# Kernel optimization log

Measured on AMD Instinct MI355X. Metric: run time of the kernel, lower is better.

The kernel has to match this reference:

```python
import jax, jax.numpy as jnp
from jax import lax
import numpy as np

T, B, IN, H = 192, 16, 256, 256


def setup_inputs() -> dict:
    key = jax.random.key(0)
    ks = jax.random.split(key, 8)
    s = 0.05  # small init scale to keep gates well-conditioned
    return {
        "x": jax.random.normal(ks[0], (T, B, IN), dtype=jnp.float32),
        # shared LSTM (PyTorch gate order i,f,g,o)
        "W_ih": jax.random.normal(ks[1], (4 * H, IN), dtype=jnp.float32) * s,
        "W_hh": jax.random.normal(ks[2], (4 * H, H), dtype=jnp.float32) * s,
        "b_lstm": jnp.zeros((4 * H,), dtype=jnp.float32),
        # additive attention: Ws: (IN+2H)->H, Us: H->1
        "Ws_w": jax.random.normal(ks[3], (H, IN + 2 * H), dtype=jnp.float32) * s,
        "Ws_b": jnp.zeros((H,), dtype=jnp.float32),
        "Us_w": jax.random.normal(ks[4], (1, H), dtype=jnp.float32) * s,
        "Us_b": jnp.zeros((1,), dtype=jnp.float32),
        # task-specific message LSTM cell: gates from concat(x_t, Rt, h_prev)
        "Wc": jax.random.normal(ks[5], (4 * H, IN + 2 * H), dtype=jnp.float32) * s,
        "bc": jnp.zeros((4 * H,), dtype=jnp.float32),
        "TASK": 0,
    }


def _lstm_gates(pre, c):
    i, f, g, o = jnp.split(pre, 4, axis=-1)
    i = jax.nn.sigmoid(i)
    f = jax.nn.sigmoid(f)
    g = jnp.tanh(g)
    o = jax.nn.sigmoid(o)
    c_new = f * c + i * g
    h_new = o * jnp.tanh(c_new)
    return h_new, c_new


def reference(x, W_ih, W_hh, b_lstm, Ws_w, Ws_b, Us_w, Us_b, Wc, bc, TASK):
    t_len, b, _ = x.shape
    h = W_hh.shape[1]

    h0 = jnp.zeros((b, h), x.dtype)

    # ---- shared LSTM over time ----
    def shared_step(carry, xt):
        hh, cc = carry
        pre = xt @ W_ih.T + hh @ W_hh.T + b_lstm
        hh, cc = _lstm_gates(pre, cc)
        return (hh, cc), hh

    (_, _), hs = lax.scan(shared_step, (h0, h0), x)  # hs: [T,B,H]

    # ---- per-timestep additive attention + message LSTM cell ----
    def task_step(carry, xt):
        hh, cc = carry
        h_task = jnp.broadcast_to(hh[None], (t_len, b, h))
        cat = jnp.concatenate([hs, h_task, x], axis=-1)          # [T,B,IN+2H]
        score = jnp.tanh(cat @ Ws_w.T + Ws_b) @ Us_w.T + Us_b    # [T,B,1]
        att = jax.nn.softmax(score, axis=0)                       # over time
        Rt = jnp.sum(att * hs, axis=0)                            # [B,H]
        pre = jnp.concatenate([xt, Rt, hh], axis=-1) @ Wc.T + bc
        hh, cc = _lstm_gates(pre, cc)
        return (hh, cc), hh

    (_, _), outs = lax.scan(task_step, (h0, h0), x)  # [T,B,H]
    return jnp.transpose(outs, (1, 0, 2))  # [B,T,H] (torch.stack axis=1)
```

## Files before the change

### kernel.cpp

```cpp
#include <hip/hip_runtime.h>
#include <hip/hip_fp16.h>

#define T_LEN 192

typedef unsigned long long u64;
typedef _Float16 f16x8 __attribute__((ext_vector_type(8)));
typedef float f32x4 __attribute__((ext_vector_type(4)));

#define OFF_X1F   0
#define OFF_XPRE  3145728
#define OFF_XB3   6291456
#define OFF_HSB   7077888
#define OFF_P     7864320
#define OFF_H     7921664
#define OFF_HX    7929856
#define OFF_HP    7946240
#define EXCH_WORDS 147456

#define SMEM_TASK 148736

__device__ __forceinline__ unsigned packh2(float a, float b){
  union { __half2 h; unsigned u; } v;
  v.h = __halves2half2(__float2half(a), __float2half(b));
  return v.u;
}
__device__ __forceinline__ float2 unp2(unsigned u){
  union { unsigned u32; __half2 h; } v; v.u32 = u;
  return __half22float2(v.h);
}
__device__ __forceinline__ float fdot2(unsigned a, unsigned b, float c){
#if __has_builtin(__builtin_amdgcn_fdot2)
  typedef _Float16 h2t __attribute__((ext_vector_type(2)));
  union { unsigned u; h2t h; } ua, ub;
  ua.u = a; ub.u = b;
  return __builtin_amdgcn_fdot2(ua.h, ub.h, c, false);
#else
  float2 x = unp2(a), y = unp2(b);
  return c + x.x*y.x + x.y*y.y;
#endif
}
__device__ __forceinline__ float tanh_f(float x){
  float cx = fminf(fmaxf(x, -15.f), 15.f);
  float e = __expf(2.f * cx);
  return (e - 1.f) / (e + 1.f);
}
__device__ __forceinline__ float sigm(float x){
  float cx = fminf(fmaxf(x, -30.f), 30.f);
  return 1.f / (1.f + __expf(-cx));
}

__device__ __forceinline__ u64 gld64(const u64* p){
  return __hip_atomic_load(p, __ATOMIC_RELAXED, __HIP_MEMORY_SCOPE_AGENT);
}
__device__ __forceinline__ void gst64(u64* p, u64 v){
  __hip_atomic_store(p, v, __ATOMIC_RELAXED, __HIP_MEMORY_SCOPE_AGENT);
}

__global__ __launch_bounds__(256) void initk(float* p, int n){
  int i = blockIdx.x * blockDim.x + threadIdx.x;
  int stride = gridDim.x * blockDim.x;
  for (; i < n; i += stride) p[i] = 0.f;
}

__global__ __launch_bounds__(256) void proj3m(const float* __restrict__ x,
                                              const float* __restrict__ W_ih,
                                              const float* __restrict__ b_l,
                                              const float* __restrict__ Wc,
                                              const float* __restrict__ bc,
                                              const float* __restrict__ Ws_w,
                                              const float* __restrict__ Ws_b,
                                              float* __restrict__ ws){
  __shared__ unsigned xhi[16 * 136];
  __shared__ unsigned xlo[16 * 136];
  const int bx = blockIdx.x, t = blockIdx.y, tid = threadIdx.x;

  {
    int row = tid >> 4, c0 = (tid & 15) * 16;
    const float* xp = &x[(t * 16 + row) * 256 + c0];
    #pragma unroll
    for (int i = 0; i < 8; ++i) {
      float2 v = *(const float2*)&xp[2 * i];
      _Float16 h0 = (_Float16)v.x, h1 = (_Float16)v.y;
      float l0 = v.x - (float)h0, l1 = v.y - (float)h1;
      union { _Float16 h[2]; unsigned u; } ph, pl;
      ph.h[0] = h0; ph.h[1] = h1;
      pl.h[0] = (_Float16)l0; pl.h[1] = (_Float16)l1;
      xhi[row * 136 + c0 / 2 + i] = ph.u;
      xlo[row * 136 + c0 / 2 + i] = pl.u;
    }
  }

  const int wave = tid >> 6, lane = tid & 63;
  const int b16 = lane & 15, quad = lane >> 4;
  const int n0 = bx * 64 + wave * 16;
  const float* wrow; const float* bias; int nb, mode;
  if (bx < 16)      { nb = n0;        wrow = &W_ih[(nb + b16) * 256];       bias = b_l;  mode = 0; }
  else if (bx < 32) { nb = n0 - 1024; wrow = &Wc[(nb + b16) * 768];         bias = bc;   mode = 1; }
  else              { nb = n0 - 2048; wrow = &Ws_w[(nb + b16) * 768 + 512]; bias = Ws_b; mode = 2; }

  f16x8 whi[8], wlo[8];
  #pragma unroll
  for (int kk = 0; kk < 8; ++kk) {
    const float* wp = wrow + kk * 32 + quad * 8;
    f16x8 h, l;
    #pragma unroll
    for (int j = 0; j < 8; ++j) {
      float v = wp[j];
      _Float16 hh = (_Float16)v;
      h[j] = hh; l[j] = (_Float16)(v - (float)hh);
    }
    whi[kk] = h; wlo[kk] = l;
  }
  f32x4 acc;
  #pragma unroll
  for (int r = 0; r < 4; ++r) acc[r] = bias[nb + quad * 4 + r];
  __syncthreads();

  #pragma unroll
  for (int kk = 0; kk < 8; ++kk) {
    union { uint4 u; f16x8 h; } bh, bl;
    bh.u = *(const uint4*)&xhi[b16 * 136 + kk * 16 + quad * 4];
    bl.u = *(const uint4*)&xlo[b16 * 136 + kk * 16 + quad * 4];
    acc = __builtin_amdgcn_mfma_f32_16x16x32_f16(whi[kk], bh.h, acc, 0, 0, 0);
    acc = __builtin_amdgcn_mfma_f32_16x16x32_f16(wlo[kk], bh.h, acc, 0, 0, 0);
    acc = __builtin_amdgcn_mfma_f32_16x16x32_f16(whi[kk], bl.h, acc, 0, 0, 0);
  }

  float4 res; res.x = acc[0]; res.y = acc[1]; res.z = acc[2]; res.w = acc[3];
  if (mode == 0) {
    *(float4*)&ws[OFF_X1F + (((u64)t * 64 + (n0 >> 4)) * 16 + b16) * 16 + quad * 4] = res;
  } else if (mode == 1) {
    *(float4*)&ws[OFF_XPRE + ((u64)t * 16 + b16) * 1024 + nb + quad * 4] = res;
  } else {
    *(float4*)&ws[OFF_XB3 + ((u64)t * 16 + b16) * 256 + nb + quad * 4] = res;
  }
}

__global__ __launch_bounds__(512) void lstm_kernel(const float* __restrict__ X1F,
                                                   const float* __restrict__ W_hh,
                                                   float* __restrict__ hsB,
                                                   u64* __restrict__ hx){
  __shared__ unsigned hT[16 * 136];
  const int tid = threadIdx.x;
  const int wg = blockIdx.x;
  const int wave = tid >> 6, lane = tid & 63;
  const int b16 = lane & 15, quad = lane >> 4;
  const int jb = wg * 8 + wave;
  const int peerbase = (1 - wg) * 64;

  f16x8 wf[4][8];
  #pragma unroll
  for (int g = 0; g < 4; ++g) {
    #pragma unroll
    for (int kk = 0; kk < 8; ++kk) {
      int row = g * 256 + jb * 16 + b16;
      const float* wp = &W_hh[row * 256 + kk * 32 + quad * 8];
      f16x8 v;
      #pragma unroll
      for (int j = 0; j < 8; ++j) v[j] = (_Float16)wp[j];
      wf[g][kk] = v;
    }
  }
  for (int i = tid; i < 16 * 136; i += 512) hT[i] = 0u;
  float cst[4] = {0.f, 0.f, 0.f, 0.f};
  __syncthreads();

  for (int t = 0; t < T_LEN; ++t) {
    float4 xi[4];
    #pragma unroll
    for (int g = 0; g < 4; ++g)
      xi[g] = *(const float4*)&X1F[((t * 64 + g * 16 + jb) * 16 + b16) * 16 + quad * 4];

    if (t > 0) {
      const u64* src = &hx[((u64)((t - 1) & 1)) * 2048];
      int bbq = tid >> 5, k2 = tid & 31;
      int jp0 = peerbase + 2 * k2;
      u64 v0, v1;
      for (;;) {
        v0 = gld64(&src[bbq * 128 + jp0]);
        v1 = gld64(&src[bbq * 128 + jp0 + 1]);
        if ((unsigned)v0 == (unsigned)t && (unsigned)v1 == (unsigned)t) break;
      }
      hT[bbq * 136 + jp0]     = (unsigned)(v0 >> 32);
      hT[bbq * 136 + jp0 + 1] = (unsigned)(v1 >> 32);
    }
    __syncthreads();

    f32x4 acc[4];
    #pragma unroll
    for (int g = 0; g < 4; ++g) {
      f32x4 a; a[0]=xi[g].x; a[1]=xi[g].y; a[2]=xi[g].z; a[3]=xi[g].w;
      acc[g] = a;
    }
    #pragma unroll
    for (int kk = 0; kk < 8; ++kk) {
      union { uint4 u; f16x8 h; } bv;
      bv.u = *(const uint4*)&hT[b16 * 136 + kk * 16 + quad * 4];
      #pragma unroll
      for (int g = 0; g < 4; ++g)
        acc[g] = __builtin_amdgcn_mfma_f32_16x16x32_f16(wf[g][kk], bv.h, acc[g], 0, 0, 0);
    }
    __syncthreads();

    float hv[4];
    #pragma unroll
    for (int r = 0; r < 4; ++r) {
      float pi = acc[0][r], pf = acc[1][r], pg = acc[2][r], po = acc[3][r];
      float cn = fmaf(sigm(pf), cst[r], sigm(pi) * tanh_f(pg));
      hv[r] = sigm(po) * tanh_f(cn);
      cst[r] = cn;
    }
    int j0 = jb * 16 + quad * 4;
    int jp = j0 >> 1;
    unsigned p01 = packh2(hv[0], hv[1]);
    unsigned p23 = packh2(hv[2], hv[3]);
    u64* dst = &hx[((u64)(t & 1)) * 2048];
    gst64(&dst[b16 * 128 + jp],     ((u64)p01 << 32) | (unsigned)(t + 1));
    gst64(&dst[b16 * 128 + jp + 1], ((u64)p23 << 32) | (unsigned)(t + 1));
    *(float4*)&hsB[(b16 * 192 + t) * 256 + j0] = make_float4(hv[0], hv[1], hv[2], hv[3]);
    hT[b16 * 136 + jp]     = p01;
    hT[b16 * 136 + jp + 1] = p23;
  }
}

__global__ __launch_bounds__(1024) void task_kernel(
    const float* __restrict__ xb3, const float* __restrict__ xpre,
    const float* __restrict__ hsB, const float* __restrict__ Us_w,
    const float* __restrict__ Us_b, const float* __restrict__ Wc,
    const float* __restrict__ Ws_w,
    u64* __restrict__ Pbuf, u64* __restrict__ Hbuf, u64* __restrict__ HPbuf,
    float* __restrict__ out){
  extern __shared__ char smem[];
  unsigned* hsL  = (unsigned*)smem;
  unsigned* Ws1L = (unsigned*)(smem + 99072);
  float*    baseS= (float*)(smem + 115584);
  unsigned* WcH  = (unsigned*)smem;
  unsigned* Ws2P = (unsigned*)(smem + 65536);
  float* prel    = (float*)(smem + 82944);
  float* eel     = (float*)(smem + 89600);
  unsigned* h2l  = (unsigned*)(smem + 90368);
  unsigned* h2own= (unsigned*)(smem + 90880);
  float* hterml  = (float*)(smem + 90944);
  float* usl     = (float*)(smem + 91072);
  float* msc     = (float*)(smem + 91200);
  unsigned* G2   = (unsigned*)(smem + 99072);

  const int tid = threadIdx.x;
  const int bb = blockIdx.x & 15;
  const int s  = blockIdx.x >> 4;

  for (int idx = tid; idx < 24576; idx += 1024) {
    int tp = idx >> 7, k2 = idx & 127;
    const float* hp = &hsB[(bb * 192 + tp) * 256 + 2 * k2];
    hsL[tp * 129 + k2] = packh2(hp[0], hp[1]);
  }
  for (int idx = tid; idx < 4096; idx += 1024) {
    int c = idx >> 7, k2 = idx & 127;
    const float* wp = &Ws_w[(32 * s + c) * 768 + 2 * k2];
    Ws1L[c * 129 + k2] = packh2(wp[0], wp[1]);
  }
  __syncthreads();
  {
    int c = tid & 31, g = tid >> 5;
    float a6[6];
    #pragma unroll
    for (int j = 0; j < 6; ++j)
      a6[j] = xb3[((g * 6 + j) * 16 + bb) * 256 + 32 * s + c];
    for (int k2 = 0; k2 < 128; ++k2) {
      unsigned wv = Ws1L[c * 129 + k2];
      #pragma unroll
      for (int j = 0; j < 6; ++j)
        a6[j] = fdot2(wv, hsL[(g * 6 + j) * 129 + k2], a6[j]);
    }
    #pragma unroll
    for (int j = 0; j < 6; ++j)
      baseS[(g * 6 + j) * 33 + c] = a6[j];
  }
  __syncthreads();
  unsigned bs4[4] = {0u, 0u, 0u, 0u};
  if (tid < 768) {
    int tp = tid >> 2, q = tid & 3;
    #pragma unroll
    for (int j2 = 0; j2 < 4; ++j2)
      bs4[j2] = packh2(baseS[tp * 33 + q * 8 + 2 * j2],
                       baseS[tp * 33 + q * 8 + 2 * j2 + 1]);
  }
  __syncthreads();
  {
    int l = tid & 127, tg = tid >> 7;
    int row = (l >> 5) * 256 + 32 * s + (l & 31);
    const float* wr = &Wc[row * 768 + 256];
    float acc[24];
    #pragma unroll
    for (int i = 0; i < 24; ++i) acc[i] = 0.f;
    for (int kc = 0; kc < 128; kc += 16) {
      unsigned wv[16];
      #pragma unroll
      for (int i = 0; i < 16; ++i) {
        float2 wp2 = *(const float2*)&wr[2 * (kc + i)];
        wv[i] = packh2(wp2.x, wp2.y);
      }
      #pragma unroll
      for (int tt = 0; tt < 24; ++tt) {
        const unsigned* hp = &hsL[(tg * 24 + tt) * 129 + kc];
        float a = acc[tt];
        #pragma unroll
        for (int i = 0; i < 16; ++i) a = fdot2(wv[i], hp[i], a);
        acc[tt] = a;
      }
    }
    #pragma unroll
    for (int i = 0; i < 12; ++i)
      G2[l * 97 + tg * 12 + i] = packh2(acc[2 * i], acc[2 * i + 1]);
  }
  __syncthreads();
  for (int idx = tid; idx < 16384; idx += 1024) {
    int j = idx & 3, l = (idx >> 2) & 127, k2q = idx >> 9;
    int k2 = k2q * 4 + j;
    int row = (l >> 5) * 256 + 32 * s + (l & 31);
    const float* wp = &Wc[row * 768 + 512 + 2 * k2];
    WcH[idx] = packh2(wp[0], wp[1]);
  }
  for (int idx = tid; idx < 4096; idx += 1024) {
    int c = idx >> 4, j = idx & 15;
    const float* wp = &Ws_w[c * 768 + 256 + 2 * (16 * s + j)];
    Ws2P[c * 17 + j] = packh2(wp[0], wp[1]);
  }
  if (tid < 32) usl[tid] = Us_w[32 * s + tid];
  const float usb = Us_b[0];
  __syncthreads();

  u64* Pb  = Pbuf + (bb * 8) * 192;
  u64* Hb  = Hbuf + bb * 256;
  u64* HPb = HPbuf + (bb * 8) * 256;
  const uint4* wp4 = (const uint4*)WcH;
  const uint4* av4 = (const uint4*)h2l;
  float creg = 0.f;

  for (int t = 0; t < T_LEN; ++t) {
    const unsigned seq = (unsigned)(t + 1);
    float xp0 = 0.f, xp1 = 0.f, xp2 = 0.f, xp3 = 0.f;
    if (tid < 32) {
      const float* xq = &xpre[(t * 16 + bb) * 1024 + 32 * s + tid];
      xp0 = xq[0]; xp1 = xq[256]; xp2 = xq[512]; xp3 = xq[768];
    }
    if (t > 0) {
      if (tid < 256) {
        int c = tid >> 3, sp = tid & 7;
        u64 v;
        do { v = gld64(&HPb[sp * 256 + 32 * s + c]); } while ((unsigned)v != (unsigned)t);
        float a = __uint_as_float((unsigned)(v >> 32));
        a += __shfl_xor(a, 1); a += __shfl_xor(a, 2); a += __shfl_xor(a, 4);
        if (sp == 0) hterml[c] = a;
      } else if (tid < 512) {
        int col = tid - 256;
        u64 v;
        do { v = gld64(&Hb[col]); } while ((unsigned)v != (unsigned)t);
        float hvv = __uint_as_float((unsigned)(v >> 32));
        float hp_ = __shfl_xor(hvv, 1);
        if ((col & 1) == 0) h2l[col >> 1] = packh2(hvv, hp_);
      }
    } else {
      if (tid < 32) hterml[tid] = 0.f;
      if (tid < 128) h2l[tid] = 0u;
    }
    __syncthreads();
    if (tid < 768) {
      int tp = tid >> 2, q = tid & 3;
      float p = 0.f;
      #pragma unroll
      for (int m = 0; m < 4; ++m) {
        float2 bv = unp2(bs4[m]);
        int c0 = q * 8 + 2 * m;
        p += usl[c0]     * tanh_f(bv.x + hterml[c0]);
        p += usl[c0 + 1] * tanh_f(bv.y + hterml[c0 + 1]);
      }
      p += __shfl_xor(p, 1);
      p += __shfl_xor(p, 2);
      if ((tid & 3) == 0)
        gst64(&Pb[s * 192 + tp], ((u64)__float_as_uint(p) << 32) | seq);
    }
    {
      int l = tid & 127, kq = tid >> 7;
      float a = 0.f;
      #pragma unroll
      for (int i = 0; i < 4; ++i) {
        uint4 w4 = wp4[(kq * 4 + i) * 128 + l];
        uint4 a4 = av4[kq * 4 + i];
        a = fdot2(w4.x, a4.x, a); a = fdot2(w4.y, a4.y, a);
        a = fdot2(w4.z, a4.z, a); a = fdot2(w4.w, a4.w, a);
      }
      prel[l * 13 + kq] = a;
    }
    if (tid < 192) {
      u64 v[8];
      for (;;) {
        bool ok = true;
        #pragma unroll
        for (int sp = 0; sp < 8; ++sp) {
          v[sp] = gld64(&Pb[sp * 192 + tid]);
          ok &= ((unsigned)v[sp] == seq);
        }
        if (ok) break;
      }
      float sum = 0.f;
      #pragma unroll
      for (int sp = 0; sp < 8; ++sp) sum += __uint_as_float((unsigned)(v[sp] >> 32));
      eel[tid] = __expf(sum + usb);
    }
    __syncthreads();
    if (tid < 64) {
      float aa = eel[tid] + eel[tid + 64] + eel[tid + 128];
      #pragma unroll
      for (int off = 32; off >= 1; off >>= 1) aa += __shfl_xor(aa, off);
      if (tid == 0) msc[0] = 1.f / aa;
    }
    if (tid >= 512) {
      int l = (tid - 512) & 127, tq = (tid - 512) >> 7;
      const unsigned* gp = &G2[l * 97 + tq * 24];
      const float2* ep = (const float2*)&eel[tq * 48];
      float a = 0.f;
      #pragma unroll
      for (int i = 0; i < 24; ++i) {
        float2 g = unp2(gp[i]);
        float2 e = ep[i];
        a = fmaf(g.x, e.x, a); a = fmaf(g.y, e.y, a);
      }
      prel[l * 13 + 8 + tq] = a;
    }
    __syncthreads();
    if (tid < 32) {
      float m = msc[0];
      float pr[4];
      #pragma unroll
      for (int g = 0; g < 4; ++g) {
        const float* pp = &prel[(g * 32 + tid) * 13];
        float hsum = pp[0] + pp[1] + pp[2] + pp[3] + pp[4] + pp[5] + pp[6] + pp[7];
        float gsum = pp[8] + pp[9] + pp[10] + pp[11];
        pr[g] = hsum + m * gsum;
      }
      pr[0] += xp0; pr[1] += xp1; pr[2] += xp2; pr[3] += xp3;
      float cn = fmaf(sigm(pr[1]), creg, sigm(pr[0]) * tanh_f(pr[2]));
      float hh = sigm(pr[3]) * tanh_f(cn);
      creg = cn;
      gst64(&Hb[32 * s + tid], ((u64)__float_as_uint(hh) << 32) | seq);
      out[(bb * 192 + t) * 256 + 32 * s + tid] = hh;
      float hp_ = __shfl_xor(hh, 1);
      if ((tid & 1) == 0) h2own[tid >> 1] = packh2(hh, hp_);
    }
    __syncthreads();
    if (tid < 256) {
      float a = 0.f;
      const unsigned* wp = &Ws2P[tid * 17];
      #pragma unroll
      for (int j = 0; j < 16; ++j) a = fdot2(wp[j], h2own[j], a);
      gst64(&HPb[s * 256 + tid], ((u64)__float_as_uint(a) << 32) | seq);
    }
  }
}

extern "C" void kernel_launch(void* const* d_in, const int* in_sizes, int n_in,
                              void* d_out, int out_size, void* d_ws, size_t ws_size,
                              hipStream_t stream) {
  (void)in_sizes; (void)n_in; (void)out_size; (void)ws_size;
  const float* x    = (const float*)d_in[0];
  const float* W_ih = (const float*)d_in[1];
  const float* W_hh = (const float*)d_in[2];
  const float* b_l  = (const float*)d_in[3];
  const float* Ws_w = (const float*)d_in[4];
  const float* Ws_b = (const float*)d_in[5];
  const float* Us_w = (const float*)d_in[6];
  const float* Us_b = (const float*)d_in[7];
  const float* Wc   = (const float*)d_in[8];
  const float* bc   = (const float*)d_in[9];
  float* out = (float*)d_out;
  float* ws = (float*)d_ws;

  hipFuncSetAttribute((const void*)task_kernel,
                      hipFuncAttributeMaxDynamicSharedMemorySize, 160 * 1024);

  initk<<<64, 256, 0, stream>>>(ws + OFF_P, EXCH_WORDS);

  proj3m<<<dim3(36, 192), 256, 0, stream>>>(x, W_ih, b_l, Wc, bc, Ws_w, Ws_b, ws);

  lstm_kernel<<<2, 512, 0, stream>>>(ws + OFF_X1F, W_hh, ws + OFF_HSB,
                                     (u64*)(ws + OFF_HX));

  task_kernel<<<128, 1024, SMEM_TASK, stream>>>(
      ws + OFF_XB3, ws + OFF_XPRE, ws + OFF_HSB, Us_w, Us_b, Wc, Ws_w,
      (u64*)(ws + OFF_P), (u64*)(ws + OFF_H), (u64*)(ws + OFF_HP), out);
}
```

Measured before the change: 1.653 ms.

## Replace cross-block MFMA LSTM with per-batch independent blocks using fdot2

The shared LSTM recurrence previously ran on 2 workgroups that exchanged hidden state through global memory with spin-wait flags every timestep. It now runs one 1024-thread block per batch element, with no inter-block sync. Each thread computes one gate pre-activation via fp16 fdot2 against a pre-converted, transposed fp16 W_hh that is streamed from global or L2 each step. The projection kernel also processes two timesteps per block so its weight fragments are reused, and the X1F layout changes accordingly. This removes the cross-block polling latency, but every block now re-reads the 512KB fp16 weight matrix each step instead of keeping it in registers.

```diff
diff --git a/kernel.cpp b/kernel.cpp
--- a/kernel.cpp
+++ b/kernel.cpp
@@ -13,8 +13,8 @@
 #define OFF_HSB   7077888
 #define OFF_P     7864320
 #define OFF_H     7921664
-#define OFF_HX    7929856
 #define OFF_HP    7946240
+#define OFF_WHH   8011776
 #define EXCH_WORDS 147456
 
 #define SMEM_TASK 148736
@@ -62,6 +62,17 @@
   for (; i < n; i += stride) p[i] = 0.f;
 }
 
+__global__ __launch_bounds__(512) void whhc(const float* __restrict__ W_hh,
+                                            uint4* __restrict__ w4t){
+  int idx = blockIdx.x * 512 + threadIdx.x;
+  int j = idx >> 5, ko = idx & 31;
+  const float* wp = &W_hh[j * 256 + ko * 8];
+  uint4 v;
+  v.x = packh2(wp[0], wp[1]); v.y = packh2(wp[2], wp[3]);
+  v.z = packh2(wp[4], wp[5]); v.w = packh2(wp[6], wp[7]);
+  w4t[ko * 1024 + j] = v;
+}
+
 __global__ __launch_bounds__(256) void proj3m(const float* __restrict__ x,
                                               const float* __restrict__ W_ih,
                                               const float* __restrict__ b_l,
@@ -70,13 +81,14 @@
                                               const float* __restrict__ Ws_w,
                                               const float* __restrict__ Ws_b,
                                               float* __restrict__ ws){
-  __shared__ unsigned xhi[16 * 136];
-  __shared__ unsigned xlo[16 * 136];
-  const int bx = blockIdx.x, t = blockIdx.y, tid = threadIdx.x;
-
-  {
+  __shared__ unsigned xhi[2][16 * 136];
+  __shared__ unsigned xlo[2][16 * 136];
+  const int bx = blockIdx.x, t0 = blockIdx.y * 2, tid = threadIdx.x;
+
+  #pragma unroll
+  for (int tt = 0; tt < 2; ++tt) {
     int row = tid >> 4, c0 = (tid & 15) * 16;
-    const float* xp = &x[(t * 16 + row) * 256 + c0];
+    const float* xp = &x[((t0 + tt) * 16 + row) * 256 + c0];
     #pragma unroll
     for (int i = 0; i < 8; ++i) {
       float2 v = *(const float2*)&xp[2 * i];
@@ -85,8 +97,8 @@
       union { _Float16 h[2]; unsigned u; } ph, pl;
       ph.h[0] = h0; ph.h[1] = h1;
       pl.h[0] = (_Float16)l0; pl.h[1] = (_Float16)l1;
-      xhi[row * 136 + c0 / 2 + i] = ph.u;
-      xlo[row * 136 + c0 / 2 + i] = pl.u;
+      xhi[tt][row * 136 + c0 / 2 + i] = ph.u;
+      xlo[tt][row * 136 + c0 / 2 + i] = pl.u;
     }
   }
 
@@ -111,115 +123,73 @@
     }
     whi[kk] = h; wlo[kk] = l;
   }
-  f32x4 acc;
+  f32x4 acc[2];
   #pragma unroll
-  for (int r = 0; r < 4; ++r) acc[r] = bias[nb + quad * 4 + r];
+  for (int tt = 0; tt < 2; ++tt)
+    #pragma unroll
+    for (int r = 0; r < 4; ++r) acc[tt][r] = bias[nb + quad * 4 + r];
   __syncthreads();
 
   #pragma unroll
   for (int kk = 0; kk < 8; ++kk) {
-    union { uint4 u; f16x8 h; } bh, bl;
-    bh.u = *(const uint4*)&xhi[b16 * 136 + kk * 16 + quad * 4];
-    bl.u = *(const uint4*)&xlo[b16 * 136 + kk * 16 + quad * 4];
-    acc = __builtin_amdgcn_mfma_f32_16x16x32_f16(whi[kk], bh.h, acc, 0, 0, 0);
-    acc = __builtin_amdgcn_mfma_f32_16x16x32_f16(wlo[kk], bh.h, acc, 0, 0, 0);
-    acc = __builtin_amdgcn_mfma_f32_16x16x32_f16(whi[kk], bl.h, acc, 0, 0, 0);
-  }
-
-  float4 res; res.x = acc[0]; res.y = acc[1]; res.z = acc[2]; res.w = acc[3];
-  if (mode == 0) {
-    *(float4*)&ws[OFF_X1F + (((u64)t * 64 + (n0 >> 4)) * 16 + b16) * 16 + quad * 4] = res;
-  } else if (mode == 1) {
-    *(float4*)&ws[OFF_XPRE + ((u64)t * 16 + b16) * 1024 + nb + quad * 4] = res;
-  } else {
-    *(float4*)&ws[OFF_XB3 + ((u64)t * 16 + b16) * 256 + nb + quad * 4] = res;
-  }
-}
-
-__global__ __launch_bounds__(512) void lstm_kernel(const float* __restrict__ X1F,
-                                                   const float* __restrict__ W_hh,
-                                                   float* __restrict__ hsB,
-                                                   u64* __restrict__ hx){
-  __shared__ unsigned hT[16 * 136];
+    #pragma unroll
+    for (int tt = 0; tt < 2; ++tt) {
+      union { uint4 u; f16x8 h; } bh, bl;
+      bh.u = *(const uint4*)&xhi[tt][b16 * 136 + kk * 16 + quad * 4];
+      bl.u = *(const uint4*)&xlo[tt][b16 * 136 + kk * 16 + quad * 4];
+      acc[tt] = __builtin_amdgcn_mfma_f32_16x16x32_f16(whi[kk], bh.h, acc[tt], 0, 0, 0);
+      acc[tt] = __builtin_amdgcn_mfma_f32_16x16x32_f16(wlo[kk], bh.h, acc[tt], 0, 0, 0);
+      acc[tt] = __builtin_amdgcn_mfma_f32_16x16x32_f16(whi[kk], bl.h, acc[tt], 0, 0, 0);
+    }
+  }
+
+  #pragma unroll
+  for (int tt = 0; tt < 2; ++tt) {
+    int t = t0 + tt;
+    float4 res; res.x = acc[tt][0]; res.y = acc[tt][1]; res.z = acc[tt][2]; res.w = acc[tt][3];
+    if (mode == 0) {
+      *(float4*)&ws[OFF_X1F + ((u64)t * 16 + b16) * 1024 + nb + quad * 4] = res;
+    } else if (mode == 1) {
+      *(float4*)&ws[OFF_XPRE + ((u64)t * 16 + b16) * 1024 + nb + quad * 4] = res;
+    } else {
+      *(float4*)&ws[OFF_XB3 + ((u64)t * 16 + b16) * 256 + nb + quad * 4] = res;
+    }
+  }
+}
+
+__global__ __launch_bounds__(1024) void lstm_b(const float* __restrict__ x1,
+                                               const uint4* __restrict__ w4t,
+                                               float* __restrict__ hsB){
+  __shared__ uint4 h4l[32];
+  __shared__ float pre[1024];
   const int tid = threadIdx.x;
-  const int wg = blockIdx.x;
-  const int wave = tid >> 6, lane = tid & 63;
-  const int b16 = lane & 15, quad = lane >> 4;
-  const int jb = wg * 8 + wave;
-  const int peerbase = (1 - wg) * 64;
-
-  f16x8 wf[4][8];
-  #pragma unroll
-  for (int g = 0; g < 4; ++g) {
-    #pragma unroll
-    for (int kk = 0; kk < 8; ++kk) {
-      int row = g * 256 + jb * 16 + b16;
-      const float* wp = &W_hh[row * 256 + kk * 32 + quad * 8];
-      f16x8 v;
-      #pragma unroll
-      for (int j = 0; j < 8; ++j) v[j] = (_Float16)wp[j];
-      wf[g][kk] = v;
-    }
-  }
-  for (int i = tid; i < 16 * 136; i += 512) hT[i] = 0u;
-  float cst[4] = {0.f, 0.f, 0.f, 0.f};
-  __syncthreads();
+  const int bb = blockIdx.x;
+  float cst = 0.f;
+  if (tid < 32) h4l[tid] = make_uint4(0u, 0u, 0u, 0u);
+  __syncthreads();
+  const uint4* wrow = w4t + tid;
 
   for (int t = 0; t < T_LEN; ++t) {
-    float4 xi[4];
-    #pragma unroll
-    for (int g = 0; g < 4; ++g)
-      xi[g] = *(const float4*)&X1F[((t * 64 + g * 16 + jb) * 16 + b16) * 16 + quad * 4];
-
-    if (t > 0) {
-      const u64* src = &hx[((u64)((t - 1) & 1)) * 2048];
-      int bbq = tid >> 5, k2 = tid & 31;
-      int jp0 = peerbase + 2 * k2;
-      u64 v0, v1;
-      for (;;) {
-        v0 = gld64(&src[bbq * 128 + jp0]);
-        v1 = gld64(&src[bbq * 128 + jp0 + 1]);
-        if ((unsigned)v0 == (unsigned)t && (unsigned)v1 == (unsigned)t) break;
-      }
-      hT[bbq * 136 + jp0]     = (unsigned)(v0 >> 32);
-      hT[bbq * 136 + jp0 + 1] = (unsigned)(v1 >> 32);
-    }
-    __syncthreads();
-
-    f32x4 acc[4];
-    #pragma unroll
-    for (int g = 0; g < 4; ++g) {
-      f32x4 a; a[0]=xi[g].x; a[1]=xi[g].y; a[2]=xi[g].z; a[3]=xi[g].w;
-      acc[g] = a;
-    }
-    #pragma unroll
-    for (int kk = 0; kk < 8; ++kk) {
-      union { uint4 u; f16x8 h; } bv;
-      bv.u = *(const uint4*)&hT[b16 * 136 + kk * 16 + quad * 4];
-      #pragma unroll
-      for (int g = 0; g < 4; ++g)
-        acc[g] = __builtin_amdgcn_mfma_f32_16x16x32_f16(wf[g][kk], bv.h, acc[g], 0, 0, 0);
-    }
-    __syncthreads();
-
-    float hv[4];
-    #pragma unroll
-    for (int r = 0; r < 4; ++r) {
-      float pi = acc[0][r], pf = acc[1][r], pg = acc[2][r], po = acc[3][r];
-      float cn = fmaf(sigm(pf), cst[r], sigm(pi) * tanh_f(pg));
-      hv[r] = sigm(po) * tanh_f(cn);
-      cst[r] = cn;
-    }
-    int j0 = jb * 16 + quad * 4;
-    int jp = j0 >> 1;
-    unsigned p01 = packh2(hv[0], hv[1]);
-    unsigned p23 = packh2(hv[2], hv[3]);
-    u64* dst = &hx[((u64)(t & 1)) * 2048];
-    gst64(&dst[b16 * 128 + jp],     ((u64)p01 << 32) | (unsigned)(t + 1));
-    gst64(&dst[b16 * 128 + jp + 1], ((u64)p23 << 32) | (unsigned)(t + 1));
-    *(float4*)&hsB[(b16 * 192 + t) * 256 + j0] = make_float4(hv[0], hv[1], hv[2], hv[3]);
-    hT[b16 * 136 + jp]     = p01;
-    hT[b16 * 136 + jp + 1] = p23;
+    float a = x1[(t * 16 + bb) * 1024 + tid];
+    #pragma unroll 8
+    for (int ko = 0; ko < 32; ++ko) {
+      uint4 w = wrow[ko * 1024];
+      uint4 hv = h4l[ko];
+      a = fdot2(w.x, hv.x, a); a = fdot2(w.y, hv.y, a);
+      a = fdot2(w.z, hv.z, a); a = fdot2(w.w, hv.w, a);
+    }
+    pre[tid] = a;
+    __syncthreads();
+    if (tid < 256) {
+      float pi = pre[tid], pf = pre[tid + 256], pg = pre[tid + 512], po = pre[tid + 768];
+      float cn = fmaf(sigm(pf), cst, sigm(pi) * tanh_f(pg));
+      float hh = sigm(po) * tanh_f(cn);
+      cst = cn;
+      hsB[(bb * 192 + t) * 256 + tid] = hh;
+      float hp_ = __shfl_xor(hh, 1);
+      if ((tid & 1) == 0) ((unsigned*)h4l)[tid >> 1] = packh2(hh, hp_);
+    }
+    __syncthreads();
   }
 }
 
@@ -481,10 +451,12 @@
 
   initk<<<64, 256, 0, stream>>>(ws + OFF_P, EXCH_WORDS);
 
-  proj3m<<<dim3(36, 192), 256, 0, stream>>>(x, W_ih, b_l, Wc, bc, Ws_w, Ws_b, ws);
-
-  lstm_kernel<<<2, 512, 0, stream>>>(ws + OFF_X1F, W_hh, ws + OFF_HSB,
-                                     (u64*)(ws + OFF_HX));
+  whhc<<<64, 512, 0, stream>>>(W_hh, (uint4*)(ws + OFF_WHH));
+
+  proj3m<<<dim3(36, 96), 256, 0, stream>>>(x, W_ih, b_l, Wc, bc, Ws_w, Ws_b, ws);
+
+  lstm_b<<<16, 1024, 0, stream>>>(ws + OFF_X1F, (const uint4*)(ws + OFF_WHH),
+                                  ws + OFF_HSB);
 
   task_kernel<<<128, 1024, SMEM_TASK, stream>>>(
       ws + OFF_XB3, ws + OFF_XPRE, ws + OFF_HSB, Us_w, Us_b, Wc, Ws_w,
```

Result: slower. 1.866 ms (+12.9%).

## Overlap Wc/Ws projections with the recurrent LSTM and split its h-matmul

Applied to the files above, without the earlier changes.

The input projection kernel is split. The W_ih part stays as its own kernel, now processing two timesteps per block to reuse the converted weights. The Wc and Ws projections move into extra blocks of the LSTM launch, so they run on otherwise idle CUs while the two recurrent blocks step through time. Inside the recurrence, the MFMA half that uses the block's own hidden slice is issued before spinning on the peer's slice, which hides part of the exchange latency. This adds barrier and ordering changes, and it depends on the two LSTM blocks being scheduled alongside the 960 projection blocks, which must not starve them.

```diff
diff --git a/kernel.cpp b/kernel.cpp
--- a/kernel.cpp
+++ b/kernel.cpp
@@ -62,21 +62,18 @@
   for (; i < n; i += stride) p[i] = 0.f;
 }
 
-__global__ __launch_bounds__(256) void proj3m(const float* __restrict__ x,
-                                              const float* __restrict__ W_ih,
-                                              const float* __restrict__ b_l,
-                                              const float* __restrict__ Wc,
-                                              const float* __restrict__ bc,
-                                              const float* __restrict__ Ws_w,
-                                              const float* __restrict__ Ws_b,
-                                              float* __restrict__ ws){
-  __shared__ unsigned xhi[16 * 136];
-  __shared__ unsigned xlo[16 * 136];
-  const int bx = blockIdx.x, t = blockIdx.y, tid = threadIdx.x;
-
-  {
+__global__ __launch_bounds__(256) void proj_x1(const float* __restrict__ x,
+                                               const float* __restrict__ W_ih,
+                                               const float* __restrict__ b_l,
+                                               float* __restrict__ ws){
+  __shared__ unsigned xhi[2][16 * 136];
+  __shared__ unsigned xlo[2][16 * 136];
+  const int bx = blockIdx.x, t0 = blockIdx.y * 2, tid = threadIdx.x;
+
+  #pragma unroll
+  for (int tt = 0; tt < 2; ++tt) {
     int row = tid >> 4, c0 = (tid & 15) * 16;
-    const float* xp = &x[(t * 16 + row) * 256 + c0];
+    const float* xp = &x[((t0 + tt) * 16 + row) * 256 + c0];
     #pragma unroll
     for (int i = 0; i < 8; ++i) {
       float2 v = *(const float2*)&xp[2 * i];
@@ -85,18 +82,15 @@
       union { _Float16 h[2]; unsigned u; } ph, pl;
       ph.h[0] = h0; ph.h[1] = h1;
       pl.h[0] = (_Float16)l0; pl.h[1] = (_Float16)l1;
-      xhi[row * 136 + c0 / 2 + i] = ph.u;
-      xlo[row * 136 + c0 / 2 + i] = pl.u;
+      xhi[tt][row * 136 + c0 / 2 + i] = ph.u;
+      xlo[tt][row * 136 + c0 / 2 + i] = pl.u;
     }
   }
 
   const int wave = tid >> 6, lane = tid & 63;
   const int b16 = lane & 15, quad = lane >> 4;
   const int n0 = bx * 64 + wave * 16;
-  const float* wrow; const float* bias; int nb, mode;
-  if (bx < 16)      { nb = n0;        wrow = &W_ih[(nb + b16) * 256];       bias = b_l;  mode = 0; }
-  else if (bx < 32) { nb = n0 - 1024; wrow = &Wc[(nb + b16) * 768];         bias = bc;   mode = 1; }
-  else              { nb = n0 - 2048; wrow = &Ws_w[(nb + b16) * 768 + 512]; bias = Ws_b; mode = 2; }
+  const float* wrow = &W_ih[(n0 + b16) * 256];
 
   f16x8 whi[8], wlo[8];
   #pragma unroll
@@ -111,42 +105,128 @@
     }
     whi[kk] = h; wlo[kk] = l;
   }
-  f32x4 acc;
+  f32x4 acc[2];
   #pragma unroll
-  for (int r = 0; r < 4; ++r) acc[r] = bias[nb + quad * 4 + r];
+  for (int tt = 0; tt < 2; ++tt)
+    #pragma unroll
+    for (int r = 0; r < 4; ++r) acc[tt][r] = b_l[n0 + quad * 4 + r];
   __syncthreads();
 
   #pragma unroll
   for (int kk = 0; kk < 8; ++kk) {
-    union { uint4 u; f16x8 h; } bh, bl;
-    bh.u = *(const uint4*)&xhi[b16 * 136 + kk * 16 + quad * 4];
-    bl.u = *(const uint4*)&xlo[b16 * 136 + kk * 16 + quad * 4];
-    acc = __builtin_amdgcn_mfma_f32_16x16x32_f16(whi[kk], bh.h, acc, 0, 0, 0);
-    acc = __builtin_amdgcn_mfma_f32_16x16x32_f16(wlo[kk], bh.h, acc, 0, 0, 0);
-    acc = __builtin_amdgcn_mfma_f32_16x16x32_f16(whi[kk], bl.h, acc, 0, 0, 0);
-  }
-
-  float4 res; res.x = acc[0]; res.y = acc[1]; res.z = acc[2]; res.w = acc[3];
-  if (mode == 0) {
+    #pragma unroll
+    for (int tt = 0; tt < 2; ++tt) {
+      union { uint4 u; f16x8 h; } bh, bl;
+      bh.u = *(const uint4*)&xhi[tt][b16 * 136 + kk * 16 + quad * 4];
+      bl.u = *(const uint4*)&xlo[tt][b16 * 136 + kk * 16 + quad * 4];
+      acc[tt] = __builtin_amdgcn_mfma_f32_16x16x32_f16(whi[kk], bh.h, acc[tt], 0, 0, 0);
+      acc[tt] = __builtin_amdgcn_mfma_f32_16x16x32_f16(wlo[kk], bh.h, acc[tt], 0, 0, 0);
+      acc[tt] = __builtin_amdgcn_mfma_f32_16x16x32_f16(whi[kk], bl.h, acc[tt], 0, 0, 0);
+    }
+  }
+
+  #pragma unroll
+  for (int tt = 0; tt < 2; ++tt) {
+    int t = t0 + tt;
+    float4 res; res.x = acc[tt][0]; res.y = acc[tt][1]; res.z = acc[tt][2]; res.w = acc[tt][3];
     *(float4*)&ws[OFF_X1F + (((u64)t * 64 + (n0 >> 4)) * 16 + b16) * 16 + quad * 4] = res;
-  } else if (mode == 1) {
-    *(float4*)&ws[OFF_XPRE + ((u64)t * 16 + b16) * 1024 + nb + quad * 4] = res;
-  } else {
-    *(float4*)&ws[OFF_XB3 + ((u64)t * 16 + b16) * 256 + nb + quad * 4] = res;
-  }
-}
-
-__global__ __launch_bounds__(512) void lstm_kernel(const float* __restrict__ X1F,
-                                                   const float* __restrict__ W_hh,
-                                                   float* __restrict__ hsB,
-                                                   u64* __restrict__ hx){
+  }
+}
+
+__global__ __launch_bounds__(512) void lstm_fused(const float* __restrict__ X1F,
+                                                  const float* __restrict__ W_hh,
+                                                  float* __restrict__ hsB,
+                                                  u64* __restrict__ hx,
+                                                  const float* __restrict__ x,
+                                                  const float* __restrict__ Wc,
+                                                  const float* __restrict__ bc,
+                                                  const float* __restrict__ Ws_w,
+                                                  const float* __restrict__ Ws_b,
+                                                  float* __restrict__ ws){
   __shared__ unsigned hT[16 * 136];
+  __shared__ unsigned xhi[2][16 * 136];
+  __shared__ unsigned xlo[2][16 * 136];
+  const int bid = blockIdx.x;
   const int tid = threadIdx.x;
-  const int wg = blockIdx.x;
   const int wave = tid >> 6, lane = tid & 63;
   const int b16 = lane & 15, quad = lane >> 4;
+
+  if (bid >= 2) {
+    const int idx2 = bid - 2;
+    const int pb = idx2 / 96, tpair = idx2 % 96, t0 = tpair * 2;
+    {
+      int tt = tid >> 8, sid = tid & 255;
+      int row = sid >> 4, c0 = (sid & 15) * 16;
+      const float* xp = &x[((t0 + tt) * 16 + row) * 256 + c0];
+      #pragma unroll
+      for (int i = 0; i < 8; ++i) {
+        float2 v = *(const float2*)&xp[2 * i];
+        _Float16 h0 = (_Float16)v.x, h1 = (_Float16)v.y;
+        float l0 = v.x - (float)h0, l1 = v.y - (float)h1;
+        union { _Float16 h[2]; unsigned u; } ph, pl;
+        ph.h[0] = h0; ph.h[1] = h1;
+        pl.h[0] = (_Float16)l0; pl.h[1] = (_Float16)l1;
+        xhi[tt][row * 136 + c0 / 2 + i] = ph.u;
+        xlo[tt][row * 136 + c0 / 2 + i] = pl.u;
+      }
+    }
+    const int bxx = 16 + pb * 2 + (wave >> 2);
+    const int wv = wave & 3;
+    const int n0g = bxx * 64 + wv * 16;
+    const float* wrow; const float* bias; int nb, mode;
+    if (bxx < 32) { nb = n0g - 1024; wrow = &Wc[(nb + b16) * 768];         bias = bc;   mode = 1; }
+    else          { nb = n0g - 2048; wrow = &Ws_w[(nb + b16) * 768 + 512]; bias = Ws_b; mode = 2; }
+
+    f16x8 whi[8], wlo[8];
+    #pragma unroll
+    for (int kk = 0; kk < 8; ++kk) {
+      const float* wp = wrow + kk * 32 + quad * 8;
+      f16x8 h, l;
+      #pragma unroll
+      for (int j = 0; j < 8; ++j) {
+        float v = wp[j];
+        _Float16 hh = (_Float16)v;
+        h[j] = hh; l[j] = (_Float16)(v - (float)hh);
+      }
+      whi[kk] = h; wlo[kk] = l;
+    }
+    f32x4 acc[2];
+    #pragma unroll
+    for (int tt = 0; tt < 2; ++tt)
+      #pragma unroll
+      for (int r = 0; r < 4; ++r) acc[tt][r] = bias[nb + quad * 4 + r];
+    __syncthreads();
+
+    #pragma unroll
+    for (int kk = 0; kk < 8; ++kk) {
+      #pragma unroll
+      for (int tt = 0; tt < 2; ++tt) {
+        union { uint4 u; f16x8 h; } bh, bl;
+        bh.u = *(const uint4*)&xhi[tt][b16 * 136 + kk * 16 + quad * 4];
+        bl.u = *(const uint4*)&xlo[tt][b16 * 136 + kk * 16 + quad * 4];
+        acc[tt] = __builtin_amdgcn_mfma_f32_16x16x32_f16(whi[kk], bh.h, acc[tt], 0, 0, 0);
+        acc[tt] = __builtin_amdgcn_mfma_f32_16x16x32_f16(wlo[kk], bh.h, acc[tt], 0, 0, 0);
+        acc[tt] = __builtin_amdgcn_mfma_f32_16x16x32_f16(whi[kk], bl.h, acc[tt], 0, 0, 0);
+      }
+    }
+    #pragma unroll
+    for (int tt = 0; tt < 2; ++tt) {
+      int t = t0 + tt;
+      float4 res; res.x = acc[tt][0]; res.y = acc[tt][1]; res.z = acc[tt][2]; res.w = acc[tt][3];
+      if (mode == 1) {
+        *(float4*)&ws[OFF_XPRE + ((u64)t * 16 + b16) * 1024 + nb + quad * 4] = res;
+      } else {
+        *(float4*)&ws[OFF_XB3 + ((u64)t * 16 + b16) * 256 + nb + quad * 4] = res;
+      }
+    }
+    return;
+  }
+
+  const int wg = bid;
   const int jb = wg * 8 + wave;
   const int peerbase = (1 - wg) * 64;
+  const int ownk0 = wg * 4;
+  const int peerk0 = (1 - wg) * 4;
 
   f16x8 wf[4][8];
   #pragma unroll
@@ -170,6 +250,20 @@
     #pragma unroll
     for (int g = 0; g < 4; ++g)
       xi[g] = *(const float4*)&X1F[((t * 64 + g * 16 + jb) * 16 + b16) * 16 + quad * 4];
+
+    f32x4 acc[4];
+    #pragma unroll
+    for (int g = 0; g < 4; ++g) { f32x4 z = {0.f, 0.f, 0.f, 0.f}; acc[g] = z; }
+
+    #pragma unroll
+    for (int kk2 = 0; kk2 < 4; ++kk2) {
+      int kk = ownk0 + kk2;
+      union { uint4 u; f16x8 h; } bv;
+      bv.u = *(const uint4*)&hT[b16 * 136 + kk * 16 + quad * 4];
+      #pragma unroll
+      for (int g = 0; g < 4; ++g)
+        acc[g] = __builtin_amdgcn_mfma_f32_16x16x32_f16(wf[g][kk], bv.h, acc[g], 0, 0, 0);
+    }
 
     if (t > 0) {
       const u64* src = &hx[((u64)((t - 1) & 1)) * 2048];
@@ -186,26 +280,23 @@
     }
     __syncthreads();
 
-    f32x4 acc[4];
-    #pragma unroll
-    for (int g = 0; g < 4; ++g) {
-      f32x4 a; a[0]=xi[g].x; a[1]=xi[g].y; a[2]=xi[g].z; a[3]=xi[g].w;
-      acc[g] = a;
-    }
-    #pragma unroll
-    for (int kk = 0; kk < 8; ++kk) {
+    #pragma unroll
+    for (int kk2 = 0; kk2 < 4; ++kk2) {
+      int kk = peerk0 + kk2;
       union { uint4 u; f16x8 h; } bv;
       bv.u = *(const uint4*)&hT[b16 * 136 + kk * 16 + quad * 4];
       #pragma unroll
       for (int g = 0; g < 4; ++g)
         acc[g] = __builtin_amdgcn_mfma_f32_16x16x32_f16(wf[g][kk], bv.h, acc[g], 0, 0, 0);
     }
-    __syncthreads();
 
     float hv[4];
     #pragma unroll
     for (int r = 0; r < 4; ++r) {
-      float pi = acc[0][r], pf = acc[1][r], pg = acc[2][r], po = acc[3][r];
+      float pi = acc[0][r] + ((const float*)&xi[0])[r];
+      float pf = acc[1][r] + ((const float*)&xi[1])[r];
+      float pg = acc[2][r] + ((const float*)&xi[2])[r];
+      float po = acc[3][r] + ((const float*)&xi[3])[r];
       float cn = fmaf(sigm(pf), cst[r], sigm(pi) * tanh_f(pg));
       hv[r] = sigm(po) * tanh_f(cn);
       cst[r] = cn;
@@ -220,6 +311,7 @@
     *(float4*)&hsB[(b16 * 192 + t) * 256 + j0] = make_float4(hv[0], hv[1], hv[2], hv[3]);
     hT[b16 * 136 + jp]     = p01;
     hT[b16 * 136 + jp + 1] = p23;
+    __syncthreads();
   }
 }
 
@@ -481,10 +573,11 @@
 
   initk<<<64, 256, 0, stream>>>(ws + OFF_P, EXCH_WORDS);
 
-  proj3m<<<dim3(36, 192), 256, 0, stream>>>(x, W_ih, b_l, Wc, bc, Ws_w, Ws_b, ws);
-
-  lstm_kernel<<<2, 512, 0, stream>>>(ws + OFF_X1F, W_hh, ws + OFF_HSB,
-                                     (u64*)(ws + OFF_HX));
+  proj_x1<<<dim3(16, 96), 256, 0, stream>>>(x, W_ih, b_l, ws);
+
+  lstm_fused<<<962, 512, 0, stream>>>(ws + OFF_X1F, W_hh, ws + OFF_HSB,
+                                      (u64*)(ws + OFF_HX),
+                                      x, Wc, bc, Ws_w, Ws_b, ws);
 
   task_kernel<<<128, 1024, SMEM_TASK, stream>>>(
       ws + OFF_XB3, ws + OFF_XPRE, ws + OFF_HSB, Us_w, Us_b, Wc, Ws_w,
```

Measured after the change: 2.876 ms. 73.9% more time.
